# Kernel tuning notes

Hardware: AMD Instinct MI355X
Metric: run time of the kernel (lower is better)

Reference implementation:

```python
import jax, jax.numpy as jnp
import numpy as np

NEG = -1e30  # log-space 'zero'
BLANK = 0


def setup_inputs() -> dict:
    key = jax.random.key(0)
    T, B, V, L = 1000, 32, 2048, 64
    k1, k2 = jax.random.split(key)
    acts = jax.random.normal(k1, (T, B, V), dtype=jnp.float32)
    # concatenated labels, one sequence of length L per example, blank=0 excluded
    labels = jax.random.randint(k2, (B * L,), 1, V, dtype=jnp.int32)
    act_lens = jnp.full((B,), T, dtype=jnp.int32)
    label_lens = jnp.full((B,), L, dtype=jnp.int32)
    return {"acts": acts, "labels": labels, "act_lens": act_lens, "label_lens": label_lens}


def _ctc_total_cost(acts, labels, act_lens, label_lens):
    # acts: (T, B, V) raw activations; warp-ctc applies softmax internally (blank=0).
    T, B, V = acts.shape
    L = labels.shape[0] // B  # uniform label length (sum(label_lens) == len(labels))
    S = 2 * L + 1
    labels2d = labels.reshape(B, L)
    # extended label sequence: blank, l1, blank, l2, ..., blank  -> (B, S)
    ext = jnp.zeros((B, S), dtype=jnp.int32).at[:, 1::2].set(labels2d)
    # transitions from s-2 allowed only for non-blank differing from ext[s-2]
    ext_m2 = jnp.concatenate([jnp.full((B, 2), -1, dtype=jnp.int32), ext[:, :-2]], axis=1)
    allow2 = (ext != BLANK) & (ext != ext_m2)  # (B, S)

    logp = jax.nn.log_softmax(acts, axis=-1)  # (T, B, V)
    # gather log-probs of extended labels: (T, B, S)
    lp_ext = jnp.take_along_axis(logp, jnp.broadcast_to(ext[None], (T, B, S)), axis=2)

    # alpha init at t=0: only s=0 (blank) and s=1 (first label)
    alpha0 = jnp.full((B, S), NEG, dtype=acts.dtype)
    alpha0 = alpha0.at[:, 0].set(lp_ext[0, :, 0]).at[:, 1].set(lp_ext[0, :, 1])

    def step(alpha, xs):
        t, lp_t = xs  # lp_t: (B, S)
        a1 = jnp.concatenate([jnp.full((B, 1), NEG, alpha.dtype), alpha[:, :-1]], axis=1)
        a2 = jnp.concatenate([jnp.full((B, 2), NEG, alpha.dtype), alpha[:, :-2]], axis=1)
        a2 = jnp.where(allow2, a2, NEG)
        new = jnp.logaddexp(jnp.logaddexp(alpha, a1), a2) + lp_t
        # freeze alpha for sequences that have already ended
        new = jnp.where((t < act_lens)[:, None], new, alpha)
        return new, None

    alphaT, _ = jax.lax.scan(step, alpha0, (jnp.arange(1, T), lp_ext[1:]))

    # terminal states: last blank (s=2*label_len) and last label (s=2*label_len-1)
    s_last = (2 * label_lens).astype(jnp.int32)  # (B,)
    a_end1 = jnp.take_along_axis(alphaT, s_last[:, None], axis=1)[:, 0]
    a_end2 = jnp.take_along_axis(alphaT, (s_last - 1)[:, None], axis=1)[:, 0]
    loss_b = -jnp.logaddexp(a_end1, a_end2)  # (B,)
    # size_average=False, length_average=False -> plain sum, returned as shape (1,)
    return jnp.sum(loss_b)[None]


def reference(acts, labels, act_lens, label_lens):
    return _ctc_total_cost(acts, labels, act_lens, label_lens)
```

## Files before the change

kernel.cpp:

```cpp
#include <hip/hip_runtime.h>
#include <stdint.h>

#define LOG2E  1.4426950408889634f
#define LN2    0.6931471805599453f

typedef float v4f __attribute__((ext_vector_type(4)));

__device__ __forceinline__ float dpp_shr1_z(float x) {
  int r = __builtin_amdgcn_update_dpp(0, __float_as_int(x), 0x138, 0xf, 0xf, true);
  return __int_as_float(r);
}

template <int CTRL>
__device__ __forceinline__ float dpp_max(float v) {
  int r = __builtin_amdgcn_update_dpp(0, __float_as_int(v), CTRL, 0xf, 0xf, true);
  return fmaxf(v, __int_as_float(r));
}

__device__ __forceinline__ float wave_max_uniform(float v) {
  v = dpp_max<0x111>(v);
  v = dpp_max<0x112>(v);
  v = dpp_max<0x114>(v);
  v = dpp_max<0x118>(v);
  v = dpp_max<0x142>(v);
  v = dpp_max<0x143>(v);
  int gm = __builtin_amdgcn_readlane(__float_as_int(v), 63);
  return __int_as_float(gm);
}

__global__ __launch_bounds__(256) void k_prob_gather(
    const float* __restrict__ acts, const int* __restrict__ labels,
    float* __restrict__ lp, int T, int Tp, int B, int V, int L) {
  const int lane = threadIdx.x & 63;
  const uint32_t r = blockIdx.x * 4u + (threadIdx.x >> 6);
  if (r >= (uint32_t)(T * B)) return;
  const uint32_t b = r / (uint32_t)T;
  const uint32_t t = r % (uint32_t)T;
  const float* __restrict__ row = acts + ((size_t)t * (size_t)B + b) * (size_t)V;

  float mx, l2s;
  if (V == 2048) {
    const float4* row4 = (const float4*)row;
    float vals[32];
    mx = -3.0e38f;
#pragma unroll
    for (int q = 0; q < 8; ++q) {
      float4 v = row4[lane + (q << 6)];
      vals[q*4+0] = v.x; vals[q*4+1] = v.y; vals[q*4+2] = v.z; vals[q*4+3] = v.w;
      mx = fmaxf(mx, fmaxf(fmaxf(v.x, v.y), fmaxf(v.z, v.w)));
    }
#pragma unroll
    for (int off = 32; off >= 1; off >>= 1) mx = fmaxf(mx, __shfl_xor(mx, off, 64));
    float s = 0.0f;
#pragma unroll
    for (int k = 0; k < 32; ++k) s += exp2f((vals[k] - mx) * LOG2E);
#pragma unroll
    for (int off = 32; off >= 1; off >>= 1) s += __shfl_xor(s, off, 64);
    l2s = log2f(s);
  } else {
    float m = -3.0e38f, s = 0.0f;
    for (int i = lane; i < V; i += 64) {
      float x = row[i];
      float m2 = fmaxf(m, x);
      s = s * exp2f((m - m2) * LOG2E) + exp2f((x - m2) * LOG2E);
      m = m2;
    }
#pragma unroll
    for (int off = 32; off >= 1; off >>= 1) {
      float mo = __shfl_xor(m, off, 64), so = __shfl_xor(s, off, 64);
      float m2 = fmaxf(m, mo);
      s = s * exp2f((m - m2) * LOG2E) + so * exp2f((mo - m2) * LOG2E);
      m = m2;
    }
    mx = m;
    l2s = log2f(s);
  }

  float* __restrict__ out = lp + (size_t)b * (size_t)(L + 1) * (size_t)Tp;
  if (lane < L) {
    int lab = labels[b * (uint32_t)L + lane];
    out[(size_t)(1 + lane) * Tp + t] = exp2f((row[lab] - mx) * LOG2E - l2s);
  }
  if (lane == 0) out[t] = exp2f((row[0] - mx) * LOG2E - l2s);
}

__global__ __launch_bounds__(64, 1) void k_ctc_fwd(
    const float* __restrict__ lp, const int* __restrict__ labels,
    const int* __restrict__ act_lens, const int* __restrict__ label_lens,
    float* __restrict__ loss, int T, int Tp, int B, int L) {
  const int b = blockIdx.x;
  const int lane = threadIdx.x;
  const int Tact = __builtin_amdgcn_readfirstlane(min(act_lens[b], T));
  const int ll   = __builtin_amdgcn_readfirstlane(min(label_lens[b], L));

  const float* __restrict__ chb = lp + (size_t)b * (size_t)(L + 1) * (size_t)Tp;
  const int lclamp = (lane < L) ? lane : (L - 1);
  const float* __restrict__ chl = chb + (size_t)(1 + lclamp) * (size_t)Tp;

  int lab_i = (lane < L) ? labels[(size_t)b * L + lane] : 0;
  int lab_p = (lane >= 1 && lane - 1 < L) ? labels[(size_t)b * L + lane - 1] : -1;
  const bool allow2 = (lane >= 1) && (lab_i != 0) && (lab_i != lab_p);

  __shared__ float A_[132];

  v4f r0, r1, r2, r3;
  v4f d0, d1, d2, d3;
  float4 qb0, qb1, qb2, qb3;
  float4 nb0, nb1, nb2, nb3;
  int acc_e = 0;

  asm volatile("s_waitcnt vmcnt(0) lgkmcnt(0)" ::: "memory");
  __builtin_amdgcn_sched_barrier(0);

#define LOADR(tt) { int tc = (tt); if (tc > Tp - 16) tc = Tp - 16;           \
    const float* p_ = chl + tc;                                              \
    asm volatile("global_load_dwordx4 %0, %4, off\n\t"                       \
                 "global_load_dwordx4 %1, %4, off offset:16\n\t"             \
                 "global_load_dwordx4 %2, %4, off offset:32\n\t"             \
                 "global_load_dwordx4 %3, %4, off offset:48"                 \
                 : "=&v"(r0), "=&v"(r1), "=&v"(r2), "=&v"(r3) : "v"(p_)); }

#define WAITR asm volatile("s_waitcnt vmcnt(0)"                              \
                 : "+v"(r0), "+v"(r1), "+v"(r2), "+v"(r3));

#define COPYD { d0 = r0; d1 = r1; d2 = r2; d3 = r3; }

#define LOADB(D, tt) { int tc = (tt); if (tc > Tp - 16) tc = Tp - 16;        \
    const float4* pb4 = (const float4*)(chb + tc);                           \
    D##0 = pb4[0]; D##1 = pb4[1]; D##2 = pb4[2]; D##3 = pb4[3]; }

#define ST(PB, PL) { float pa = dpp_shr1_z(s1);                              \
    float cc = allow2 ? pa : 0.0f;                                           \
    float n0 = (s0 + pa) * (PB);                                             \
    float n1 = ((s0 + s1) + cc) * (PL);                                      \
    float n2 = (s2 + s1) * (PB);                                             \
    s0 = n0; s1 = n1; s2 = n2; }

#define RESC { float gm = wave_max_uniform(fmaxf(fmaxf(s0, s1), s2));        \
    int e = ((__float_as_int(gm) >> 23) & 0xff) - 127;                       \
    acc_e += e;                                                              \
    float sc = __int_as_float((127 - e) << 23);                              \
    s0 *= sc; s1 *= sc; s2 *= sc; }

#define STG(PB, PL, tt) { if ((tt) >= 1 && (tt) < Tact) ST(PB, PL) }

#define WIN16 {                                                              \
    ST(qb0.x, d0.x) ST(qb0.y, d0.y) ST(qb0.z, d0.z) ST(qb0.w, d0.w) RESC     \
    ST(qb1.x, d1.x) ST(qb1.y, d1.y) ST(qb1.z, d1.z) ST(qb1.w, d1.w) RESC     \
    ST(qb2.x, d2.x) ST(qb2.y, d2.y) ST(qb2.z, d2.z) ST(qb2.w, d2.w) RESC     \
    ST(qb3.x, d3.x) ST(qb3.y, d3.y) ST(qb3.z, d3.z) ST(qb3.w, d3.w) RESC }

#define WIN16G(tb) {                                                         \
    STG(qb0.x, d0.x, (tb)+0)  STG(qb0.y, d0.y, (tb)+1)                       \
    STG(qb0.z, d0.z, (tb)+2)  STG(qb0.w, d0.w, (tb)+3)  RESC                 \
    STG(qb1.x, d1.x, (tb)+4)  STG(qb1.y, d1.y, (tb)+5)                       \
    STG(qb1.z, d1.z, (tb)+6)  STG(qb1.w, d1.w, (tb)+7)  RESC                 \
    STG(qb2.x, d2.x, (tb)+8)  STG(qb2.y, d2.y, (tb)+9)                       \
    STG(qb2.z, d2.z, (tb)+10) STG(qb2.w, d2.w, (tb)+11) RESC                 \
    STG(qb3.x, d3.x, (tb)+12) STG(qb3.y, d3.y, (tb)+13)                      \
    STG(qb3.z, d3.z, (tb)+14) STG(qb3.w, d3.w, (tb)+15) RESC }

#define SWAPB { qb0 = nb0; qb1 = nb1; qb2 = nb2; qb3 = nb3; }

  LOADR(0)
  LOADB(qb, 0)
  LOADB(nb, 16)
  WAITR
  COPYD
  LOADR(16)

  float s0 = (lane == 0) ? qb0.x : 0.0f;
  float s1 = (lane == 0) ? d0.x  : 0.0f;
  float s2 = 0.0f;

  WIN16G(0)
  SWAPB LOADB(nb, 32)
  int t0 = 16;

  while (t0 + 16 <= Tact) {
    WAITR
    COPYD
    LOADR(t0 + 16)
    WIN16
    SWAPB LOADB(nb, t0 + 32)
    t0 += 16;
  }

  if (t0 < Tact) {
    WAITR
    COPYD
    WIN16G(t0)
  }

#undef LOADR
#undef WAITR
#undef COPYD
#undef LOADB
#undef ST
#undef RESC
#undef STG
#undef WIN16
#undef WIN16G
#undef SWAPB

  A_[2 * lane] = s0;
  A_[2 * lane + 1] = s1;
  if (lane == 63) A_[128] = s2;
  __syncthreads();
  if (lane == 0) {
    int sl = 2 * ll;
    float a1 = A_[sl];
    float a2 = (sl >= 1) ? A_[sl - 1] : 0.0f;
    loss[b] = -(logf(a1 + a2) + (float)acc_e * LN2);
  }
}

__global__ __launch_bounds__(64) void k_sum(const float* __restrict__ loss,
                                            float* __restrict__ out, int B) {
  int lane = threadIdx.x;
  float s = 0.0f;
  for (int i = lane; i < B; i += 64) s += loss[i];
#pragma unroll
  for (int off = 32; off >= 1; off >>= 1) s += __shfl_xor(s, off, 64);
  if (lane == 0) out[0] = s;
}

extern "C" void kernel_launch(void* const* d_in, const int* in_sizes, int n_in,
                              void* d_out, int out_size, void* d_ws, size_t ws_size,
                              hipStream_t stream) {
  const float* acts       = (const float*)d_in[0];
  const int*   labels     = (const int*)d_in[1];
  const int*   act_lens   = (const int*)d_in[2];
  const int*   label_lens = (const int*)d_in[3];

  const int B = in_sizes[2];
  const int L = in_sizes[1] / B;
  const int T = 1000;
  const int V = (int)((long long)in_sizes[0] / ((long long)T * (long long)B));
  const int Tp = (T + 31) & ~31;

  float* lp    = (float*)d_ws;
  float* lossb = lp + (size_t)B * (size_t)(L + 1) * (size_t)Tp;

  k_prob_gather<<<dim3((T * B + 3) / 4), dim3(256), 0, stream>>>(
      acts, labels, lp, T, Tp, B, V, L);
  k_ctc_fwd<<<dim3(B), dim3(64), 0, stream>>>(lp, labels, act_lens, label_lens,
                                              lossb, T, Tp, B, L);
  k_sum<<<dim3(1), dim3(64), 0, stream>>>(lossb, (float*)d_out, B);
}
```

Measured before the change: 126.1 us.

## Process two batch elements per wave in CTC forward with deferred rescaling

```diff
diff --git a/kernel.cpp b/kernel.cpp
--- a/kernel.cpp
+++ b/kernel.cpp
@@ -3,6 +3,7 @@
 
 #define LOG2E  1.4426950408889634f
 #define LN2    0.6931471805599453f
+#define BIAS_E 32
 
 typedef float v4f __attribute__((ext_vector_type(4)));
 
@@ -88,79 +89,134 @@
     const float* __restrict__ lp, const int* __restrict__ labels,
     const int* __restrict__ act_lens, const int* __restrict__ label_lens,
     float* __restrict__ loss, int T, int Tp, int B, int L) {
-  const int b = blockIdx.x;
+  const int bA = blockIdx.x;
+  const int nP = (B + 1) >> 1;
+  const int bBr = bA + nP;
+  const bool hasB = (bBr < B);
+  const int bB = hasB ? bBr : bA;
   const int lane = threadIdx.x;
-  const int Tact = __builtin_amdgcn_readfirstlane(min(act_lens[b], T));
-  const int ll   = __builtin_amdgcn_readfirstlane(min(label_lens[b], L));
-
-  const float* __restrict__ chb = lp + (size_t)b * (size_t)(L + 1) * (size_t)Tp;
+
+  const int TactA = __builtin_amdgcn_readfirstlane(min(act_lens[bA], T));
+  const int TactB = __builtin_amdgcn_readfirstlane(min(act_lens[bB], T));
+  const int llA   = __builtin_amdgcn_readfirstlane(min(label_lens[bA], L));
+  const int llB   = __builtin_amdgcn_readfirstlane(min(label_lens[bB], L));
+  const int Tmin = (TactA < TactB) ? TactA : TactB;
+  const int Tmax = (TactA > TactB) ? TactA : TactB;
+
+  const float* __restrict__ chbA = lp + (size_t)bA * (size_t)(L + 1) * (size_t)Tp;
+  const float* __restrict__ chbB = lp + (size_t)bB * (size_t)(L + 1) * (size_t)Tp;
   const int lclamp = (lane < L) ? lane : (L - 1);
-  const float* __restrict__ chl = chb + (size_t)(1 + lclamp) * (size_t)Tp;
-
-  int lab_i = (lane < L) ? labels[(size_t)b * L + lane] : 0;
-  int lab_p = (lane >= 1 && lane - 1 < L) ? labels[(size_t)b * L + lane - 1] : -1;
-  const bool allow2 = (lane >= 1) && (lab_i != 0) && (lab_i != lab_p);
-
-  __shared__ float A_[132];
-
-  v4f r0, r1, r2, r3;
-  v4f d0, d1, d2, d3;
-  float4 qb0, qb1, qb2, qb3;
-  float4 nb0, nb1, nb2, nb3;
-  int acc_e = 0;
+  const float* __restrict__ chlA = chbA + (size_t)(1 + lclamp) * (size_t)Tp;
+  const float* __restrict__ chlB = chbB + (size_t)(1 + lclamp) * (size_t)Tp;
+
+  int labA_i = (lane < L) ? labels[(size_t)bA * L + lane] : 0;
+  int labA_p = (lane >= 1 && lane - 1 < L) ? labels[(size_t)bA * L + lane - 1] : -1;
+  const bool allow2A = (lane >= 1) && (labA_i != 0) && (labA_i != labA_p);
+  int labB_i = (lane < L) ? labels[(size_t)bB * L + lane] : 0;
+  int labB_p = (lane >= 1 && lane - 1 < L) ? labels[(size_t)bB * L + lane - 1] : -1;
+  const bool allow2B = (lane >= 1) && (labB_i != 0) && (labB_i != labB_p);
+
+  __shared__ float A_[264];
+
+  v4f rA0, rA1, rA2, rA3, rB0, rB1, rB2, rB3;
+  v4f dA0, dA1, dA2, dA3, dB0, dB1, dB2, dB3;
+  float4 qbA0, qbA1, qbA2, qbA3, nbA0, nbA1, nbA2, nbA3;
+  float4 qbB0, qbB1, qbB2, qbB3, nbB0, nbB1, nbB2, nbB3;
+  int acc_eA = 0, pend_eA = 0;  float pend_scA = 1.0f;
+  int acc_eB = 0, pend_eB = 0;  float pend_scB = 1.0f;
 
   asm volatile("s_waitcnt vmcnt(0) lgkmcnt(0)" ::: "memory");
   __builtin_amdgcn_sched_barrier(0);
 
 #define LOADR(tt) { int tc = (tt); if (tc > Tp - 16) tc = Tp - 16;           \
-    const float* p_ = chl + tc;                                              \
-    asm volatile("global_load_dwordx4 %0, %4, off\n\t"                       \
-                 "global_load_dwordx4 %1, %4, off offset:16\n\t"             \
-                 "global_load_dwordx4 %2, %4, off offset:32\n\t"             \
-                 "global_load_dwordx4 %3, %4, off offset:48"                 \
-                 : "=&v"(r0), "=&v"(r1), "=&v"(r2), "=&v"(r3) : "v"(p_)); }
+    const float* pA_ = chlA + tc; const float* pB_ = chlB + tc;              \
+    asm volatile("global_load_dwordx4 %0, %8, off\n\t"                       \
+                 "global_load_dwordx4 %1, %8, off offset:16\n\t"             \
+                 "global_load_dwordx4 %2, %8, off offset:32\n\t"             \
+                 "global_load_dwordx4 %3, %8, off offset:48\n\t"             \
+                 "global_load_dwordx4 %4, %9, off\n\t"                       \
+                 "global_load_dwordx4 %5, %9, off offset:16\n\t"             \
+                 "global_load_dwordx4 %6, %9, off offset:32\n\t"             \
+                 "global_load_dwordx4 %7, %9, off offset:48"                 \
+                 : "=&v"(rA0), "=&v"(rA1), "=&v"(rA2), "=&v"(rA3),           \
+                   "=&v"(rB0), "=&v"(rB1), "=&v"(rB2), "=&v"(rB3)            \
+                 : "v"(pA_), "v"(pB_)); }
 
 #define WAITR asm volatile("s_waitcnt vmcnt(0)"                              \
-                 : "+v"(r0), "+v"(r1), "+v"(r2), "+v"(r3));
-
-#define COPYD { d0 = r0; d1 = r1; d2 = r2; d3 = r3; }
+    : "+v"(rA0), "+v"(rA1), "+v"(rA2), "+v"(rA3),                            \
+      "+v"(rB0), "+v"(rB1), "+v"(rB2), "+v"(rB3));
+
+#define COPYD { dA0 = rA0; dA1 = rA1; dA2 = rA2; dA3 = rA3;                  \
+                dB0 = rB0; dB1 = rB1; dB2 = rB2; dB3 = rB3; }
 
 #define LOADB(D, tt) { int tc = (tt); if (tc > Tp - 16) tc = Tp - 16;        \
-    const float4* pb4 = (const float4*)(chb + tc);                           \
-    D##0 = pb4[0]; D##1 = pb4[1]; D##2 = pb4[2]; D##3 = pb4[3]; }
-
-#define ST(PB, PL) { float pa = dpp_shr1_z(s1);                              \
-    float cc = allow2 ? pa : 0.0f;                                           \
-    float n0 = (s0 + pa) * (PB);                                             \
-    float n1 = ((s0 + s1) + cc) * (PL);                                      \
-    float n2 = (s2 + s1) * (PB);                                             \
-    s0 = n0; s1 = n1; s2 = n2; }
-
-#define RESC { float gm = wave_max_uniform(fmaxf(fmaxf(s0, s1), s2));        \
-    int e = ((__float_as_int(gm) >> 23) & 0xff) - 127;                       \
-    acc_e += e;                                                              \
-    float sc = __int_as_float((127 - e) << 23);                              \
-    s0 *= sc; s1 *= sc; s2 *= sc; }
-
-#define STG(PB, PL, tt) { if ((tt) >= 1 && (tt) < Tact) ST(PB, PL) }
-
-#define WIN16 {                                                              \
-    ST(qb0.x, d0.x) ST(qb0.y, d0.y) ST(qb0.z, d0.z) ST(qb0.w, d0.w) RESC     \
-    ST(qb1.x, d1.x) ST(qb1.y, d1.y) ST(qb1.z, d1.z) ST(qb1.w, d1.w) RESC     \
-    ST(qb2.x, d2.x) ST(qb2.y, d2.y) ST(qb2.z, d2.z) ST(qb2.w, d2.w) RESC     \
-    ST(qb3.x, d3.x) ST(qb3.y, d3.y) ST(qb3.z, d3.z) ST(qb3.w, d3.w) RESC }
-
-#define WIN16G(tb) {                                                         \
-    STG(qb0.x, d0.x, (tb)+0)  STG(qb0.y, d0.y, (tb)+1)                       \
-    STG(qb0.z, d0.z, (tb)+2)  STG(qb0.w, d0.w, (tb)+3)  RESC                 \
-    STG(qb1.x, d1.x, (tb)+4)  STG(qb1.y, d1.y, (tb)+5)                       \
-    STG(qb1.z, d1.z, (tb)+6)  STG(qb1.w, d1.w, (tb)+7)  RESC                 \
-    STG(qb2.x, d2.x, (tb)+8)  STG(qb2.y, d2.y, (tb)+9)                       \
-    STG(qb2.z, d2.z, (tb)+10) STG(qb2.w, d2.w, (tb)+11) RESC                 \
-    STG(qb3.x, d3.x, (tb)+12) STG(qb3.y, d3.y, (tb)+13)                      \
-    STG(qb3.z, d3.z, (tb)+14) STG(qb3.w, d3.w, (tb)+15) RESC }
-
-#define SWAPB { qb0 = nb0; qb1 = nb1; qb2 = nb2; qb3 = nb3; }
+    const float4* pA4 = (const float4*)(chbA + tc);                          \
+    const float4* pB4 = (const float4*)(chbB + tc);                          \
+    D##A0 = pA4[0]; D##A1 = pA4[1]; D##A2 = pA4[2]; D##A3 = pA4[3];          \
+    D##B0 = pB4[0]; D##B1 = pB4[1]; D##B2 = pB4[2]; D##B3 = pB4[3]; }
+
+#define STA(PB, PL) { float pa = dpp_shr1_z(s1A);                            \
+    float cc = allow2A ? pa : 0.0f;                                          \
+    float n0 = (s0A + pa) * (PB);                                            \
+    float n1 = ((s0A + s1A) + cc) * (PL);                                    \
+    float n2 = (s2A + s1A) * (PB);                                           \
+    s0A = n0; s1A = n1; s2A = n2; }
+
+#define STB(PB, PL) { float pa = dpp_shr1_z(s1B);                            \
+    float cc = allow2B ? pa : 0.0f;                                          \
+    float n0 = (s0B + pa) * (PB);                                            \
+    float n1 = ((s0B + s1B) + cc) * (PL);                                    \
+    float n2 = (s2B + s1B) * (PB);                                           \
+    s0B = n0; s1B = n1; s2B = n2; }
+
+#define STAB(PBA, PLA, PBB, PLB) { STA(PBA, PLA) STB(PBB, PLB) }
+
+#define RESC {                                                               \
+    s0A *= pend_scA; s1A *= pend_scA; s2A *= pend_scA; acc_eA += pend_eA;    \
+    s0B *= pend_scB; s1B *= pend_scB; s2B *= pend_scB; acc_eB += pend_eB;    \
+    float gmA = wave_max_uniform(fmaxf(fmaxf(s0A, s1A), s2A));               \
+    float gmB = wave_max_uniform(fmaxf(fmaxf(s0B, s1B), s2B));               \
+    int eA = ((__float_as_int(gmA) >> 23) & 0xff) - 127 - BIAS_E;            \
+    int eB = ((__float_as_int(gmB) >> 23) & 0xff) - 127 - BIAS_E;            \
+    if (eA < -126) eA = -126;                                                \
+    if (eB < -126) eB = -126;                                                \
+    pend_eA = eA; pend_scA = __int_as_float((127 - eA) << 23);               \
+    pend_eB = eB; pend_scB = __int_as_float((127 - eB) << 23); }
+
+#define STGAB(PBA, PLA, PBB, PLB, tt) {                                      \
+    if ((tt) >= 1 && (tt) < TactA) STA(PBA, PLA)                             \
+    if ((tt) >= 1 && (tt) < TactB) STB(PBB, PLB) }
+
+#define WIN16 {                                                                        \
+    STAB(qbA0.x, dA0.x, qbB0.x, dB0.x) STAB(qbA0.y, dA0.y, qbB0.y, dB0.y)              \
+    STAB(qbA0.z, dA0.z, qbB0.z, dB0.z) STAB(qbA0.w, dA0.w, qbB0.w, dB0.w) RESC         \
+    STAB(qbA1.x, dA1.x, qbB1.x, dB1.x) STAB(qbA1.y, dA1.y, qbB1.y, dB1.y)              \
+    STAB(qbA1.z, dA1.z, qbB1.z, dB1.z) STAB(qbA1.w, dA1.w, qbB1.w, dB1.w) RESC         \
+    STAB(qbA2.x, dA2.x, qbB2.x, dB2.x) STAB(qbA2.y, dA2.y, qbB2.y, dB2.y)              \
+    STAB(qbA2.z, dA2.z, qbB2.z, dB2.z) STAB(qbA2.w, dA2.w, qbB2.w, dB2.w) RESC         \
+    STAB(qbA3.x, dA3.x, qbB3.x, dB3.x) STAB(qbA3.y, dA3.y, qbB3.y, dB3.y)              \
+    STAB(qbA3.z, dA3.z, qbB3.z, dB3.z) STAB(qbA3.w, dA3.w, qbB3.w, dB3.w) RESC }
+
+#define WIN16G(tb) {                                                                   \
+    STGAB(qbA0.x, dA0.x, qbB0.x, dB0.x, (tb)+0)                                        \
+    STGAB(qbA0.y, dA0.y, qbB0.y, dB0.y, (tb)+1)                                        \
+    STGAB(qbA0.z, dA0.z, qbB0.z, dB0.z, (tb)+2)                                        \
+    STGAB(qbA0.w, dA0.w, qbB0.w, dB0.w, (tb)+3)  RESC                                  \
+    STGAB(qbA1.x, dA1.x, qbB1.x, dB1.x, (tb)+4)                                        \
+    STGAB(qbA1.y, dA1.y, qbB1.y, dB1.y, (tb)+5)                                        \
+    STGAB(qbA1.z, dA1.z, qbB1.z, dB1.z, (tb)+6)                                        \
+    STGAB(qbA1.w, dA1.w, qbB1.w, dB1.w, (tb)+7)  RESC                                  \
+    STGAB(qbA2.x, dA2.x, qbB2.x, dB2.x, (tb)+8)                                        \
+    STGAB(qbA2.y, dA2.y, qbB2.y, dB2.y, (tb)+9)                                        \
+    STGAB(qbA2.z, dA2.z, qbB2.z, dB2.z, (tb)+10)                                       \
+    STGAB(qbA2.w, dA2.w, qbB2.w, dB2.w, (tb)+11) RESC                                  \
+    STGAB(qbA3.x, dA3.x, qbB3.x, dB3.x, (tb)+12)                                       \
+    STGAB(qbA3.y, dA3.y, qbB3.y, dB3.y, (tb)+13)                                       \
+    STGAB(qbA3.z, dA3.z, qbB3.z, dB3.z, (tb)+14)                                       \
+    STGAB(qbA3.w, dA3.w, qbB3.w, dB3.w, (tb)+15) RESC }
+
+#define SWAPB { qbA0 = nbA0; qbA1 = nbA1; qbA2 = nbA2; qbA3 = nbA3;          \
+                qbB0 = nbB0; qbB1 = nbB1; qbB2 = nbB2; qbB3 = nbB3; }
 
   LOADR(0)
   LOADB(qb, 0)
@@ -169,15 +225,18 @@
   COPYD
   LOADR(16)
 
-  float s0 = (lane == 0) ? qb0.x : 0.0f;
-  float s1 = (lane == 0) ? d0.x  : 0.0f;
-  float s2 = 0.0f;
+  float s0A = (lane == 0) ? qbA0.x : 0.0f;
+  float s1A = (lane == 0) ? dA0.x  : 0.0f;
+  float s2A = 0.0f;
+  float s0B = (lane == 0) ? qbB0.x : 0.0f;
+  float s1B = (lane == 0) ? dB0.x  : 0.0f;
+  float s2B = 0.0f;
 
   WIN16G(0)
   SWAPB LOADB(nb, 32)
   int t0 = 16;
 
-  while (t0 + 16 <= Tact) {
+  while (t0 + 16 <= Tmin) {
     WAITR
     COPYD
     LOADR(t0 + 16)
@@ -185,33 +244,45 @@
     SWAPB LOADB(nb, t0 + 32)
     t0 += 16;
   }
-
-  if (t0 < Tact) {
+  while (t0 < Tmax) {
     WAITR
     COPYD
+    LOADR(t0 + 16)
     WIN16G(t0)
+    SWAPB LOADB(nb, t0 + 32)
+    t0 += 16;
   }
 
 #undef LOADR
 #undef WAITR
 #undef COPYD
 #undef LOADB
-#undef ST
+#undef STA
+#undef STB
+#undef STAB
 #undef RESC
-#undef STG
+#undef STGAB
 #undef WIN16
 #undef WIN16G
 #undef SWAPB
 
-  A_[2 * lane] = s0;
-  A_[2 * lane + 1] = s1;
-  if (lane == 63) A_[128] = s2;
+  A_[2 * lane] = s0A;
+  A_[2 * lane + 1] = s1A;
+  A_[132 + 2 * lane] = s0B;
+  A_[132 + 2 * lane + 1] = s1B;
+  if (lane == 63) { A_[128] = s2A; A_[132 + 128] = s2B; }
   __syncthreads();
   if (lane == 0) {
-    int sl = 2 * ll;
-    float a1 = A_[sl];
-    float a2 = (sl >= 1) ? A_[sl - 1] : 0.0f;
-    loss[b] = -(logf(a1 + a2) + (float)acc_e * LN2);
+    int slA = 2 * llA;
+    float a1 = A_[slA];
+    float a2 = (slA >= 1) ? A_[slA - 1] : 0.0f;
+    loss[bA] = -(logf(a1 + a2) + (float)acc_eA * LN2);
+    if (hasB) {
+      int slB = 2 * llB;
+      float b1 = A_[132 + slB];
+      float b2 = (slB >= 1) ? A_[132 + slB - 1] : 0.0f;
+      loss[bB] = -(logf(b1 + b2) + (float)acc_eB * LN2);
+    }
   }
 }
 
@@ -244,7 +315,7 @@
 
   k_prob_gather<<<dim3((T * B + 3) / 4), dim3(256), 0, stream>>>(
       acts, labels, lp, T, Tp, B, V, L);
-  k_ctc_fwd<<<dim3(B), dim3(64), 0, stream>>>(lp, labels, act_lens, label_lens,
-                                              lossb, T, Tp, B, L);
+  k_ctc_fwd<<<dim3((B + 1) / 2), dim3(64), 0, stream>>>(
+      lp, labels, act_lens, label_lens, lossb, T, Tp, B, L);
   k_sum<<<dim3(1), dim3(64), 0, stream>>>(lossb, (float*)d_out, B);
 }
```

New measurement: 164.3 us. +30.2%, slower.
